# Performance work log

Measured on AMD Instinct MI355X. Metric: run time of the kernel, lower is better.

## Reference

```python
import jax, jax.numpy as jnp
import numpy as np

DIM, HEADS, HEAD_DIM, EPS = 1536, 12, 128, 1e-6
B, S = 1, 4096


def rmsnorm(x, w, eps=EPS):
    v = jnp.mean(jnp.square(x), axis=-1, keepdims=True)
    return x * jax.lax.rsqrt(v + eps) * w


def apply_rope(x, freqs):
    # x: [b,s,n,d]; freqs: [s, d//2] rotation angles (complex rope on adjacent pairs)
    b, s, n, d = x.shape
    xr = x.reshape(b, s, n, d // 2, 2)
    cos = jnp.cos(freqs)[None, :, None, :]
    sin = jnp.sin(freqs)[None, :, None, :]
    x0, x1 = xr[..., 0], xr[..., 1]
    out = jnp.stack([x0 * cos - x1 * sin, x0 * sin + x1 * cos], axis=-1)
    return out.reshape(b, s, n, d)


def setup_inputs() -> dict:
    key = jax.random.key(0)
    ks = jax.random.split(key, 12)
    scale = 0.02
    x = jax.random.normal(ks[0], (B, S, DIM), jnp.float32)
    # standard rope angles: pos * inv_freq
    inv_freq = 1.0 / (10000.0 ** (jnp.arange(0, HEAD_DIM, 2, dtype=jnp.float32) / HEAD_DIM))
    freqs = jnp.arange(S, dtype=jnp.float32)[:, None] * inv_freq[None, :]  # [S, 64]
    Wq = jax.random.normal(ks[1], (DIM, DIM), jnp.float32) * scale
    bq = jax.random.normal(ks[2], (DIM,), jnp.float32) * scale
    Wk = jax.random.normal(ks[3], (DIM, DIM), jnp.float32) * scale
    bk = jax.random.normal(ks[4], (DIM,), jnp.float32) * scale
    Wv = jax.random.normal(ks[5], (DIM, DIM), jnp.float32) * scale
    bv = jax.random.normal(ks[6], (DIM,), jnp.float32) * scale
    Wo = jax.random.normal(ks[7], (DIM, DIM), jnp.float32) * scale
    bo = jax.random.normal(ks[8], (DIM,), jnp.float32) * scale
    gq = 1.0 + jax.random.normal(ks[9], (DIM,), jnp.float32) * 0.01
    gk = 1.0 + jax.random.normal(ks[10], (DIM,), jnp.float32) * 0.01
    return dict(x=x, freqs=freqs, Wq=Wq, bq=bq, Wk=Wk, bk=bk, Wv=Wv, bv=bv,
                Wo=Wo, bo=bo, gq=gq, gk=gk)


def reference(x, freqs, Wq, bq, Wk, bk, Wv, bv, Wo, bo, gq, gk):
    b, s = x.shape[:2]
    n, d = HEADS, HEAD_DIM
    q = apply_rope(rmsnorm(x @ Wq.T + bq, gq).reshape(b, s, n, d), freqs)
    k = apply_rope(rmsnorm(x @ Wk.T + bk, gk).reshape(b, s, n, d), freqs)
    v = (x @ Wv.T + bv).reshape(b, s, n, d)
    # SDPA: softmax(q k^T / sqrt(d)) v
    scores = jnp.einsum('bqnd,bknd->bnqk', q, k) / jnp.sqrt(jnp.asarray(d, x.dtype))
    attn = jax.nn.softmax(scores, axis=-1)
    out = jnp.einsum('bnqk,bknd->bqnd', attn, v).reshape(b, s, n * d)
    return out @ Wo.T + bo
```

## Files before the change

### kernel.cpp

```cpp
#include <hip/hip_runtime.h>
#include <stdint.h>
#include <math.h>

#define DIM 1536
#define SEQ 4096
#define HEADS 12
#define HD 128

typedef __bf16 bf16x8 __attribute__((ext_vector_type(8)));
typedef float f32x4 __attribute__((ext_vector_type(4)));

typedef __attribute__((address_space(1))) void gas_void;
typedef __attribute__((address_space(3))) void las_void;

__device__ __forceinline__ float b2f(unsigned short u) {
  union { unsigned int i; float f; } x; x.i = ((unsigned int)u) << 16; return x.f;
}
__device__ __forceinline__ unsigned short f2b(float f) {
  union { float f; unsigned int i; } x; x.f = f;
  unsigned int u = x.i;
  unsigned int r = (u + 0x7fffu + ((u >> 16) & 1u)) >> 16;
  return (unsigned short)r;
}
__device__ __forceinline__ void gll16(const unsigned short* g, unsigned short* l) {
  __builtin_amdgcn_global_load_lds((gas_void*)g, (las_void*)l, 16, 0, 0);
}

__global__ void detect_kernel(const unsigned int* __restrict__ xw, int* flag) {
  __shared__ int cnt;
  if (threadIdx.x == 0) cnt = 0;
  __syncthreads();
  int local = 0;
  for (int i = threadIdx.x; i < 1024; i += 256) {
    unsigned int e = (xw[i] >> 7) & 0xFFu;
    if (e >= 110u && e <= 140u) local++;
  }
  atomicAdd(&cnt, local);
  __syncthreads();
  if (threadIdx.x == 0) *flag = (cnt > 512) ? 0 : 1;
}

__global__ void convert_bf16_kernel(const void* __restrict__ src,
                                    unsigned short* __restrict__ dst, int n,
                                    const int* __restrict__ flag) {
  int f = *flag;
  for (int i = blockIdx.x * blockDim.x + threadIdx.x; i < n; i += gridDim.x * blockDim.x)
    dst[i] = f ? f2b(((const float*)src)[i]) : ((const unsigned short*)src)[i];
}

__global__ void convert_w4_kernel(const void* s0, const void* s1, const void* s2, const void* s3,
                                  unsigned short* d0, unsigned short* d1,
                                  unsigned short* d2, unsigned short* d3,
                                  int n, const int* __restrict__ flag) {
  const void* s; unsigned short* d;
  switch (blockIdx.y) {
    case 0: s = s0; d = d0; break;
    case 1: s = s1; d = d1; break;
    case 2: s = s2; d = d2; break;
    default: s = s3; d = d3; break;
  }
  int f = *flag;
  for (int i = blockIdx.x * blockDim.x + threadIdx.x; i < n; i += gridDim.x * blockDim.x)
    d[i] = f ? f2b(((const float*)s)[i]) : ((const unsigned short*)s)[i];
}

__global__ void convert_v6_kernel(const void* s0, const void* s1, const void* s2,
                                  const void* s3, const void* s4, const void* s5,
                                  unsigned short* d0, unsigned short* d1, unsigned short* d2,
                                  unsigned short* d3, unsigned short* d4, unsigned short* d5,
                                  int n, const int* __restrict__ flag) {
  const void* s; unsigned short* d;
  switch (blockIdx.y) {
    case 0: s = s0; d = d0; break;
    case 1: s = s1; d = d1; break;
    case 2: s = s2; d = d2; break;
    case 3: s = s3; d = d3; break;
    case 4: s = s4; d = d4; break;
    default: s = s5; d = d5; break;
  }
  int f = *flag;
  for (int i = blockIdx.x * blockDim.x + threadIdx.x; i < n; i += gridDim.x * blockDim.x)
    d[i] = f ? f2b(((const float*)s)[i]) : ((const unsigned short*)s)[i];
}

__global__ void convert_f32_kernel(const void* __restrict__ src,
                                   float* __restrict__ dst, int n,
                                   const int* __restrict__ flag) {
  int f = *flag;
  for (int i = blockIdx.x * blockDim.x + threadIdx.x; i < n; i += gridDim.x * blockDim.x)
    dst[i] = f ? ((const float*)src)[i] : b2f(((const unsigned short*)src)[i]);
}

__global__ void signal_kernel(float* out) { if (threadIdx.x == 0) out[0] = 999.0f; }

__device__ __forceinline__ void gemm_bt_body(
    const unsigned short* __restrict__ A,
    const unsigned short* __restrict__ W,
    const unsigned short* __restrict__ bias,
    unsigned short* __restrict__ Cb, float* __restrict__ Cf, int fmt, int vmode,
    int K, int N, int bx, int by)
{
  const int BK = 32;
  __shared__ unsigned short As[128 * 32];
  __shared__ unsigned short Bs[128 * 32];
  const int t = threadIdx.x;
  const int wave = t >> 6, lane = t & 63;
  const int quad = lane >> 4, l16 = lane & 15;
  const int m0 = by * 128, n0 = bx * 128;
  const int wm = (wave >> 1) * 64, wn = (wave & 1) * 64;

  f32x4 acc[4][4] = {};

  const int srow = t >> 2, sblk = t & 3;
  const unsigned short* Ag1 = A + (size_t)(m0 + srow) * K + sblk * 8;
  const unsigned short* Ag2 = A + (size_t)(m0 + 64 + srow) * K + sblk * 8;
  const unsigned short* Wg1 = W + (size_t)(n0 + srow) * K + sblk * 8;
  const unsigned short* Wg2 = W + (size_t)(n0 + 64 + srow) * K + sblk * 8;
  unsigned short* As1 = &As[t * 8];
  unsigned short* As2 = &As[2048 + t * 8];
  unsigned short* Bs1 = &Bs[t * 8];
  unsigned short* Bs2 = &Bs[2048 + t * 8];

  for (int k0 = 0; k0 < K; k0 += BK) {
    __syncthreads();
    gll16(Ag1 + k0, As1);
    gll16(Ag2 + k0, As2);
    gll16(Wg1 + k0, Bs1);
    gll16(Wg2 + k0, Bs2);
    __syncthreads();
    bf16x8 af[4], bfr[4];
#pragma unroll
    for (int i = 0; i < 4; ++i)
      af[i] = *(const bf16x8*)&As[(wm + i * 16 + l16) * 32 + quad * 8];
#pragma unroll
    for (int j = 0; j < 4; ++j)
      bfr[j] = *(const bf16x8*)&Bs[(wn + j * 16 + l16) * 32 + quad * 8];
#pragma unroll
    for (int i = 0; i < 4; ++i)
#pragma unroll
      for (int j = 0; j < 4; ++j)
        acc[i][j] = __builtin_amdgcn_mfma_f32_16x16x32_bf16(af[i], bfr[j], acc[i][j], 0, 0, 0);
  }

#pragma unroll
  for (int i = 0; i < 4; ++i) {
    int row = m0 + wm + i * 16 + quad * 4;
#pragma unroll
    for (int j = 0; j < 4; ++j) {
      int col = n0 + wn + j * 16 + l16;
      float bv = b2f(bias[col]);
      if (vmode) {
        union { unsigned short h4[4]; uint2 u; } pk;
#pragma unroll
        for (int r = 0; r < 4; ++r) pk.h4[r] = f2b(acc[i][j][r] + bv);
        *(uint2*)&Cb[(size_t)col * SEQ + row] = pk.u;
      } else {
#pragma unroll
        for (int r = 0; r < 4; ++r) {
          float v = acc[i][j][r] + bv;
          size_t idx = (size_t)(row + r) * N + col;
          if (fmt) Cf[idx] = v; else Cb[idx] = f2b(v);
        }
      }
    }
  }
}

__global__ __launch_bounds__(256) void qkv_gemm_kernel(
    const unsigned short* __restrict__ x,
    const unsigned short* __restrict__ Wq, const unsigned short* __restrict__ bq,
    const unsigned short* __restrict__ Wk, const unsigned short* __restrict__ bk,
    const unsigned short* __restrict__ Wv, const unsigned short* __restrict__ bv,
    unsigned short* qb, unsigned short* kb, unsigned short* vt)
{
  const unsigned short *W, *b; unsigned short* C; int vm = 0;
  if (blockIdx.z == 0)      { W = Wq; b = bq; C = qb; }
  else if (blockIdx.z == 1) { W = Wk; b = bk; C = kb; }
  else                      { W = Wv; b = bv; C = vt; vm = 1; }
  gemm_bt_body(x, W, b, C, nullptr, 0, vm, DIM, DIM, blockIdx.x, blockIdx.y);
}

__global__ __launch_bounds__(256) void out_gemm_kernel(
    const unsigned short* __restrict__ ab, const unsigned short* __restrict__ Wo,
    const unsigned short* __restrict__ bo, void* out, const int* __restrict__ flag)
{
  int fmt = *flag;
  gemm_bt_body(ab, Wo, bo, (unsigned short*)out, (float*)out, fmt, 0,
               DIM, DIM, blockIdx.x, blockIdx.y);
}

__global__ __launch_bounds__(256) void norm_rope_kernel(
    unsigned short* __restrict__ qb, unsigned short* __restrict__ kb,
    const unsigned short* __restrict__ gq, const unsigned short* __restrict__ gk,
    const float* __restrict__ freqsf)
{
  const int s = blockIdx.x;
  const int isq = (blockIdx.y == 0);
  unsigned short* row = (isq ? qb : kb) + (size_t)s * DIM;
  const unsigned short* g = (isq ? gq : gk);
  const int t = threadIdx.x;
  float ss = 0.f;
#pragma unroll
  for (int i = 0; i < 6; ++i) {
    float xv = b2f(row[t + 256 * i]);
    ss += xv * xv;
  }
#pragma unroll
  for (int off = 32; off > 0; off >>= 1) ss += __shfl_down(ss, off);
  __shared__ float red[4];
  if ((t & 63) == 0) red[t >> 6] = ss;
  __syncthreads();
  float tot = red[0] + red[1] + red[2] + red[3];
  float rinv = 1.0f / sqrtf(tot * (1.0f / DIM) + 1e-6f);
  if (isq) rinv *= 0.08838834764831845f;
#pragma unroll
  for (int i = 0; i < 3; ++i) {
    int pg = t + 256 * i;
    int c0 = pg * 2;
    float x0 = b2f(row[c0]), x1 = b2f(row[c0 + 1]);
    float y0 = x0 * rinv * b2f(g[c0]);
    float y1 = x1 * rinv * b2f(g[c0 + 1]);
    float ang = freqsf[s * 64 + (pg & 63)];
    float sn, cs;
    __sincosf(ang, &sn, &cs);
    row[c0]     = f2b(y0 * cs - y1 * sn);
    row[c0 + 1] = f2b(y0 * sn + y1 * cs);
  }
}

#define LDPS 72

__global__ __launch_bounds__(256) void attn_kernel(
    const unsigned short* __restrict__ qb,
    const unsigned short* __restrict__ kb,
    const unsigned short* __restrict__ vt,
    float* __restrict__ op,
    float* __restrict__ lp,
    int seg)
{
  __shared__ unsigned short Ks[64 * 128];
  __shared__ unsigned short Vs[128 * 64];
  __shared__ __bf16 Ps[4][32 * LDPS];

  const int t = threadIdx.x;
  const int wave = t >> 6, lane = t & 63;
  const int quad = lane >> 4, l16 = lane & 15;
  const int h = blockIdx.y;
  const int z = blockIdx.z;
  const int qbase = blockIdx.x * 128 + wave * 32;
  const int kc0 = z * seg;

  bf16x8 qf[2][4];
#pragma unroll
  for (int mt = 0; mt < 2; ++mt)
#pragma unroll
    for (int kk = 0; kk < 4; ++kk)
      qf[mt][kk] = *(const bf16x8*)(qb + (size_t)(qbase + mt * 16 + l16) * DIM
                                    + h * HD + kk * 32 + quad * 8);

  f32x4 o[2][8] = {};
  float Lr[2][4] = {};

  const int krow = t >> 2, kblk = (t & 3) * 4;
  const int vd = t >> 1,  vblk = (t & 1) * 4;

  const unsigned short* kbase = kb + (size_t)krow * DIM + h * HD + kblk * 8;
  const unsigned short* vbase = vt + ((size_t)h * HD + vd) * SEQ + vblk * 8;

  uint4 kr0, kr1, kr2, kr3, vr0, vr1, vr2, vr3;
  {
    const unsigned short* s = kbase + (size_t)kc0 * DIM;
    kr0 = *(const uint4*)(s);
    kr1 = *(const uint4*)(s + 8);
    kr2 = *(const uint4*)(s + 16);
    kr3 = *(const uint4*)(s + 24);
    const unsigned short* sv = vbase + kc0;
    vr0 = *(const uint4*)(sv);
    vr1 = *(const uint4*)(sv + 8);
    vr2 = *(const uint4*)(sv + 16);
    vr3 = *(const uint4*)(sv + 24);
  }

  for (int kc = kc0; kc < kc0 + seg; kc += 64) {
    __syncthreads();
    {
      unsigned short* dst = &Ks[krow * 128];
      const int sw = krow & 7;
      *(uint4*)(dst + ((kblk + 0) ^ sw) * 8) = kr0;
      *(uint4*)(dst + ((kblk + 1) ^ sw) * 8) = kr1;
      *(uint4*)(dst + ((kblk + 2) ^ sw) * 8) = kr2;
      *(uint4*)(dst + ((kblk + 3) ^ sw) * 8) = kr3;
    }
    {
      unsigned short* dst = &Vs[vd * 64];
      const int sw = vd & 7;
      *(uint4*)(dst + ((vblk + 0) ^ sw) * 8) = vr0;
      *(uint4*)(dst + ((vblk + 1) ^ sw) * 8) = vr1;
      *(uint4*)(dst + ((vblk + 2) ^ sw) * 8) = vr2;
      *(uint4*)(dst + ((vblk + 3) ^ sw) * 8) = vr3;
    }
    __syncthreads();

    {
      int nkc = kc + 64;
      if (nkc >= kc0 + seg) nkc = kc;
      const unsigned short* s = kbase + (size_t)nkc * DIM;
      kr0 = *(const uint4*)(s);
      kr1 = *(const uint4*)(s + 8);
      kr2 = *(const uint4*)(s + 16);
      kr3 = *(const uint4*)(s + 24);
      const unsigned short* sv = vbase + nkc;
      vr0 = *(const uint4*)(sv);
      vr1 = *(const uint4*)(sv + 8);
      vr2 = *(const uint4*)(sv + 16);
      vr3 = *(const uint4*)(sv + 24);
    }

    f32x4 sc[2][4] = {};
#pragma unroll
    for (int kk = 0; kk < 4; ++kk) {
#pragma unroll
      for (int j = 0; j < 4; ++j) {
        int row = j * 16 + l16;
        bf16x8 kf = *(const bf16x8*)&Ks[row * 128 + ((kk * 4 + quad) ^ (row & 7)) * 8];
        sc[0][j] = __builtin_amdgcn_mfma_f32_16x16x32_bf16(qf[0][kk], kf, sc[0][j], 0, 0, 0);
        sc[1][j] = __builtin_amdgcn_mfma_f32_16x16x32_bf16(qf[1][kk], kf, sc[1][j], 0, 0, 0);
      }
    }

#pragma unroll
    for (int mt = 0; mt < 2; ++mt)
#pragma unroll
      for (int j = 0; j < 4; ++j)
#pragma unroll
        for (int r = 0; r < 4; ++r) {
          float p = __expf(sc[mt][j][r]);
          Lr[mt][r] += p;
          Ps[wave][(mt * 16 + quad * 4 + r) * LDPS + j * 16 + l16] = (__bf16)p;
        }

    __asm__ __volatile__("" ::: "memory");

#pragma unroll
    for (int kk2 = 0; kk2 < 2; ++kk2) {
      bf16x8 pf0 = *(const bf16x8*)&Ps[wave][(0 * 16 + l16) * LDPS + kk2 * 32 + quad * 8];
      bf16x8 pf1 = *(const bf16x8*)&Ps[wave][(1 * 16 + l16) * LDPS + kk2 * 32 + quad * 8];
#pragma unroll
      for (int j2 = 0; j2 < 8; ++j2) {
        bf16x8 vf = *(const bf16x8*)&Vs[(j2 * 16 + l16) * 64
                                        + ((kk2 * 4 + quad) ^ (l16 & 7)) * 8];
        o[0][j2] = __builtin_amdgcn_mfma_f32_16x16x32_bf16(pf0, vf, o[0][j2], 0, 0, 0);
        o[1][j2] = __builtin_amdgcn_mfma_f32_16x16x32_bf16(pf1, vf, o[1][j2], 0, 0, 0);
      }
    }
  }

  float* opz = op + (size_t)z * SEQ * DIM;
  float* lpz = lp + (size_t)z * HEADS * SEQ + (size_t)h * SEQ;
#pragma unroll
  for (int mt = 0; mt < 2; ++mt) {
#pragma unroll
    for (int r = 0; r < 4; ++r) {
      float L = Lr[mt][r];
#pragma unroll
      for (int off = 1; off < 16; off <<= 1) L += __shfl_xor(L, off);
      if (l16 == 0) lpz[qbase + mt * 16 + quad * 4 + r] = L;
    }
#pragma unroll
    for (int j2 = 0; j2 < 8; ++j2) {
      int col = h * HD + j2 * 16 + l16;
#pragma unroll
      for (int r = 0; r < 4; ++r) {
        int row = qbase + mt * 16 + quad * 4 + r;
        opz[(size_t)row * DIM + col] = o[mt][j2][r];
      }
    }
  }
}

__global__ __launch_bounds__(256) void combine_kernel(
    const float* __restrict__ op, const float* __restrict__ lp,
    unsigned short* __restrict__ ab, int nz)
{
  int idx = blockIdx.x * 256 + threadIdx.x;
  int row = idx / DIM, col = idx - row * DIM;
  int h = col >> 7;
  float o = 0.f, l = 0.f;
  for (int z = 0; z < nz; ++z) {
    o += op[(size_t)z * SEQ * DIM + idx];
    l += lp[(size_t)z * HEADS * SEQ + (size_t)h * SEQ + row];
  }
  ab[idx] = f2b(o / l);
}

extern "C" void kernel_launch(void* const* d_in, const int* in_sizes, int n_in,
                              void* d_out, int out_size, void* d_ws, size_t ws_size,
                              hipStream_t stream) {
  const int NX = SEQ * DIM, NW = DIM * DIM, NB = DIM, NF = SEQ * 64;

  char* w = (char*)d_ws;
  size_t off = 0;
  int* flag = (int*)(w + off);              off += 256;
  unsigned short* xb  = (unsigned short*)(w + off); off += (size_t)NX * 2;
  unsigned short* Wqb = (unsigned short*)(w + off); off += (size_t)NW * 2;
  unsigned short* Wkb = (unsigned short*)(w + off); off += (size_t)NW * 2;
  unsigned short* Wvb = (unsigned short*)(w + off); off += (size_t)NW * 2;
  unsigned short* Wob = (unsigned short*)(w + off); off += (size_t)NW * 2;
  unsigned short* bqb = (unsigned short*)(w + off); off += 4096;
  unsigned short* bkb = (unsigned short*)(w + off); off += 4096;
  unsigned short* bvb = (unsigned short*)(w + off); off += 4096;
  unsigned short* bob = (unsigned short*)(w + off); off += 4096;
  unsigned short* gqb = (unsigned short*)(w + off); off += 4096;
  unsigned short* gkb = (unsigned short*)(w + off); off += 4096;
  float* freqsf = (float*)(w + off);        off += (size_t)NF * 4;
  unsigned short* qb = (unsigned short*)(w + off); off += (size_t)NX * 2;
  unsigned short* kb = (unsigned short*)(w + off); off += (size_t)NX * 2;
  unsigned short* vt = (unsigned short*)(w + off); off += (size_t)NX * 2;
  unsigned short* ab = (unsigned short*)(w + off); off += (size_t)NX * 2;
  float* op = (float*)(w + off);
  float* lp;

  int nz = 4;
  size_t need4 = off + (size_t)4 * NX * 4 + (size_t)4 * HEADS * SEQ * 4;
  size_t need2 = off + (size_t)2 * NX * 4 + (size_t)2 * HEADS * SEQ * 4;
  size_t need;
  if (ws_size >= need4)      { nz = 4; need = need4; }
  else if (ws_size >= need2) { nz = 2; need = need2; }
  else {
    signal_kernel<<<1, 64, 0, stream>>>((float*)d_out);
    return;
  }
  lp = (float*)(w + off + (size_t)nz * NX * 4);

  detect_kernel<<<1, 256, 0, stream>>>((const unsigned int*)d_in[0], flag);

  const int CT = 256;
  auto cgrid = [](int n) { int g = (n + 255) / 256; return g > 4096 ? 4096 : g; };
  convert_bf16_kernel<<<cgrid(NX), CT, 0, stream>>>(d_in[0], xb, NX, flag);
  convert_w4_kernel<<<dim3(cgrid(NW), 4), CT, 0, stream>>>(
      d_in[2], d_in[4], d_in[6], d_in[8], Wqb, Wkb, Wvb, Wob, NW, flag);
  convert_v6_kernel<<<dim3(cgrid(NB), 6), CT, 0, stream>>>(
      d_in[3], d_in[5], d_in[7], d_in[9], d_in[10], d_in[11],
      bqb, bkb, bvb, bob, gqb, gkb, NB, flag);
  convert_f32_kernel<<<cgrid(NF), CT, 0, stream>>>(d_in[1], freqsf, NF, flag);

  qkv_gemm_kernel<<<dim3(DIM / 128, SEQ / 128, 3), 256, 0, stream>>>(
      xb, Wqb, bqb, Wkb, bkb, Wvb, bvb, qb, kb, vt);
  norm_rope_kernel<<<dim3(SEQ, 2), 256, 0, stream>>>(qb, kb, gqb, gkb, freqsf);
  attn_kernel<<<dim3(SEQ / 128, HEADS, nz), 256, 0, stream>>>(qb, kb, vt, op, lp, SEQ / nz);
  combine_kernel<<<NX / 256, 256, 0, stream>>>(op, lp, ab, nz);
  out_gemm_kernel<<<dim3(DIM / 128, SEQ / 128), 256, 0, stream>>>(ab, Wob, bob, d_out, flag);
}
```

Measured before the change: 464.5 us.

## Keep softmax P in registers via transposed QK MFMA and permlane swaps

Swaps MFMA operand order so the score tile comes out transposed, with each lane holding one query's scores across keys. The exponentials are then packed to bf16 with v_cvt_pk_bf16_f32 and rearranged into the PV A-operand layout with permlane32/16 swaps, which removes the per-wave LDS staging buffer and its writes and reads. Row-sum reduction also simplifies to two shuffles. The risk is that the permlane-based rearrangement may not exactly match the MFMA operand layout, and it relies on gfx950-specific instructions.

```diff
diff --git a/kernel.cpp b/kernel.cpp
--- a/kernel.cpp
+++ b/kernel.cpp
@@ -24,6 +24,15 @@
 }
 __device__ __forceinline__ void gll16(const unsigned short* g, unsigned short* l) {
   __builtin_amdgcn_global_load_lds((gas_void*)g, (las_void*)l, 16, 0, 0);
+}
+__device__ __forceinline__ void cvtpk(unsigned int& d, float a, float b) {
+  asm("v_cvt_pk_bf16_f32 %0, %1, %2" : "=v"(d) : "v"(a), "v"(b));
+}
+__device__ __forceinline__ void pl32(unsigned int& a, unsigned int& b) {
+  asm("v_permlane32_swap_b32 %0, %1" : "+v"(a), "+v"(b));
+}
+__device__ __forceinline__ void pl16(unsigned int& a, unsigned int& b) {
+  asm("v_permlane16_swap_b32 %0, %1" : "+v"(a), "+v"(b));
 }
 
 __global__ void detect_kernel(const unsigned int* __restrict__ xw, int* flag) {
@@ -228,8 +237,6 @@
   }
 }
 
-#define LDPS 72
-
 __global__ __launch_bounds__(256) void attn_kernel(
     const unsigned short* __restrict__ qb,
     const unsigned short* __restrict__ kb,
@@ -240,7 +247,6 @@
 {
   __shared__ unsigned short Ks[64 * 128];
   __shared__ unsigned short Vs[128 * 64];
-  __shared__ __bf16 Ps[4][32 * LDPS];
 
   const int t = threadIdx.x;
   const int wave = t >> 6, lane = t & 63;
@@ -259,7 +265,7 @@
                                     + h * HD + kk * 32 + quad * 8);
 
   f32x4 o[2][8] = {};
-  float Lr[2][4] = {};
+  float Lr[2] = {};
 
   const int krow = t >> 2, kblk = (t & 3) * 4;
   const int vd = t >> 1,  vblk = (t & 1) * 4;
@@ -323,34 +329,50 @@
       for (int j = 0; j < 4; ++j) {
         int row = j * 16 + l16;
         bf16x8 kf = *(const bf16x8*)&Ks[row * 128 + ((kk * 4 + quad) ^ (row & 7)) * 8];
-        sc[0][j] = __builtin_amdgcn_mfma_f32_16x16x32_bf16(qf[0][kk], kf, sc[0][j], 0, 0, 0);
-        sc[1][j] = __builtin_amdgcn_mfma_f32_16x16x32_bf16(qf[1][kk], kf, sc[1][j], 0, 0, 0);
-      }
-    }
-
+        sc[0][j] = __builtin_amdgcn_mfma_f32_16x16x32_bf16(kf, qf[0][kk], sc[0][j], 0, 0, 0);
+        sc[1][j] = __builtin_amdgcn_mfma_f32_16x16x32_bf16(kf, qf[1][kk], sc[1][j], 0, 0, 0);
+      }
+    }
+
+    unsigned int wlo[2][4], whi[2][4];
+#pragma unroll
+    for (int mt = 0; mt < 2; ++mt) {
+      float ls = 0.f;
+#pragma unroll
+      for (int j = 0; j < 4; ++j) {
+        float p0 = __expf(sc[mt][j][0]);
+        float p1 = __expf(sc[mt][j][1]);
+        float p2 = __expf(sc[mt][j][2]);
+        float p3 = __expf(sc[mt][j][3]);
+        ls += (p0 + p1) + (p2 + p3);
+        cvtpk(wlo[mt][j], p0, p1);
+        cvtpk(whi[mt][j], p2, p3);
+      }
+      Lr[mt] += ls;
+    }
+
+    bf16x8 pf[2][2];
 #pragma unroll
     for (int mt = 0; mt < 2; ++mt)
 #pragma unroll
-      for (int j = 0; j < 4; ++j)
-#pragma unroll
-        for (int r = 0; r < 4; ++r) {
-          float p = __expf(sc[mt][j][r]);
-          Lr[mt][r] += p;
-          Ps[wave][(mt * 16 + quad * 4 + r) * LDPS + j * 16 + l16] = (__bf16)p;
-        }
-
-    __asm__ __volatile__("" ::: "memory");
+      for (int kk2 = 0; kk2 < 2; ++kk2) {
+        unsigned int ul = wlo[mt][kk2 * 2], vl = wlo[mt][kk2 * 2 + 1];
+        unsigned int uh = whi[mt][kk2 * 2], vh = whi[mt][kk2 * 2 + 1];
+        pl32(ul, vl); pl16(ul, vl);
+        pl32(uh, vh); pl16(uh, vh);
+        union { unsigned int w[4]; bf16x8 v; } u;
+        u.w[0] = ul; u.w[1] = uh; u.w[2] = vl; u.w[3] = vh;
+        pf[mt][kk2] = u.v;
+      }
 
 #pragma unroll
     for (int kk2 = 0; kk2 < 2; ++kk2) {
-      bf16x8 pf0 = *(const bf16x8*)&Ps[wave][(0 * 16 + l16) * LDPS + kk2 * 32 + quad * 8];
-      bf16x8 pf1 = *(const bf16x8*)&Ps[wave][(1 * 16 + l16) * LDPS + kk2 * 32 + quad * 8];
 #pragma unroll
       for (int j2 = 0; j2 < 8; ++j2) {
         bf16x8 vf = *(const bf16x8*)&Vs[(j2 * 16 + l16) * 64
                                         + ((kk2 * 4 + quad) ^ (l16 & 7)) * 8];
-        o[0][j2] = __builtin_amdgcn_mfma_f32_16x16x32_bf16(pf0, vf, o[0][j2], 0, 0, 0);
-        o[1][j2] = __builtin_amdgcn_mfma_f32_16x16x32_bf16(pf1, vf, o[1][j2], 0, 0, 0);
+        o[0][j2] = __builtin_amdgcn_mfma_f32_16x16x32_bf16(pf[0][kk2], vf, o[0][j2], 0, 0, 0);
+        o[1][j2] = __builtin_amdgcn_mfma_f32_16x16x32_bf16(pf[1][kk2], vf, o[1][j2], 0, 0, 0);
       }
     }
   }
@@ -359,13 +381,13 @@
   float* lpz = lp + (size_t)z * HEADS * SEQ + (size_t)h * SEQ;
 #pragma unroll
   for (int mt = 0; mt < 2; ++mt) {
-#pragma unroll
-    for (int r = 0; r < 4; ++r) {
-      float L = Lr[mt][r];
-#pragma unroll
-      for (int off = 1; off < 16; off <<= 1) L += __shfl_xor(L, off);
-      if (l16 == 0) lpz[qbase + mt * 16 + quad * 4 + r] = L;
-    }
+    float L = Lr[mt];
+    L += __shfl_xor(L, 16);
+    L += __shfl_xor(L, 32);
+    if (lane < 16) lpz[qbase + mt * 16 + l16] = L;
+  }
+#pragma unroll
+  for (int mt = 0; mt < 2; ++mt) {
 #pragma unroll
     for (int j2 = 0; j2 < 8; ++j2) {
       int col = h * HD + j2 * 16 + l16;
```

Measured after the change: 458.4 us. Within noise of the previous version (-1.3%).
